# Kernel tuning notes

Hardware: AMD Instinct MI355X
Metric: run time of the kernel (lower is better)

Reference implementation:

```python
import jax, jax.numpy as jnp
import numpy as np

B, T = 128, 1024
SERIES_IN, Y = 35, 8
H = 256
CON, BIN = 25, 10
D = SERIES_IN + Y  # 43, lstm input size


def setup_inputs() -> dict:
    key = jax.random.key(0)
    ks = jax.random.split(key, 14)
    def w(k, shape, s=0.05):
        return jax.random.normal(k, shape, dtype=jnp.float32) * s
    return {
        "x": jax.random.normal(ks[0], (B, T, D), dtype=jnp.float32),
        # DPLSTM (single layer), gate order i,f,g,o like torch
        "W_ih": w(ks[1], (4 * H, D)),
        "W_hh": w(ks[2], (4 * H, H)),
        "b_ih": w(ks[3], (4 * H,)),
        "b_hh": w(ks[4], (4 * H,)),
        # action head
        "W_afc1": w(ks[5], (H, H)),
        "b_afc1": w(ks[6], (H,)),
        "W_aout": w(ks[7], (Y, H)),
        "b_aout": w(ks[8], (Y,)),
        # outcome heads take [out, current_action] -> H+Y features
        "W_cont": w(ks[9], (2 * CON, H + Y)),
        "b_cont": w(ks[10], (2 * CON,)),
        "W_bin": w(ks[11], (BIN, H + Y)),
        "b_bin": w(ks[12], (BIN,)),
    }


def lstm(x, W_ih, W_hh, b_ih, b_hh):
    # x: [B, T, D] -> hidden states [B, T, H]; torch gate order i, f, g, o
    Hh = W_hh.shape[1]
    # precompute input projections for all timesteps (fold both biases in)
    xg = jnp.einsum("btd,gd->btg", x, W_ih) + b_ih + b_hh  # [B, T, 4H]

    def step(carry, g_t):
        h, c = carry
        gates = g_t + h @ W_hh.T  # [B, 4H]
        i, f, g, o = jnp.split(gates, 4, axis=-1)
        i = jax.nn.sigmoid(i)
        f = jax.nn.sigmoid(f)
        g = jnp.tanh(g)
        o = jax.nn.sigmoid(o)
        c = f * c + i * g
        h = o * jnp.tanh(c)
        return (h, c), h

    Bsz = x.shape[0]
    init = (jnp.zeros((Bsz, Hh), x.dtype), jnp.zeros((Bsz, Hh), x.dtype))
    _, hs = jax.lax.scan(step, init, jnp.swapaxes(xg, 0, 1))  # [T, B, H]
    return jnp.swapaxes(hs, 0, 1)


def reference(x, W_ih, W_hh, b_ih, b_hh, W_afc1, b_afc1, W_aout, b_aout,
              W_cont, b_cont, W_bin, b_bin):
    cur = x[:, :, -Y:]                                   # current action [B,T,Y]
    prev = jnp.concatenate([jnp.zeros_like(cur[:, :1]), cur[:, :-1]], axis=1)
    xin = jnp.concatenate([x[:, :, :-Y], prev], axis=-1)  # [B,T,D]
    out = lstm(xin, W_ih, W_hh, b_ih, b_hh)               # [B,T,H]
    # gradient reversal is identity in forward
    act = jax.nn.relu(out @ W_afc1.T + b_afc1) @ W_aout.T + b_aout  # [B,T,Y]
    pred = jnp.concatenate([out, cur], axis=-1)           # [B,T,H+Y]
    cont_params = pred @ W_cont.T + b_cont                # [B,T,2*CON]
    bin_params = jax.nn.sigmoid(pred @ W_bin.T + b_bin)   # [B,T,BIN]
    return cont_params, bin_params, act
```

## Files before the change

kernel.cpp:

```cpp
#include <hip/hip_runtime.h>

typedef unsigned int u32;
typedef unsigned short u16;
typedef unsigned char u8;
typedef unsigned long long u64;
typedef __attribute__((ext_vector_type(8))) short short8;
typedef __attribute__((ext_vector_type(4))) float floatx4;
typedef __attribute__((ext_vector_type(4))) int intx4;

#define TT 1024
#define BIN_OFF 6553600
#define ACT_OFF 7864320

__device__ __forceinline__ u16 f2b(float f) {
  u32 u = __builtin_bit_cast(u32, f);
  u += 0x7fffu + ((u >> 16) & 1u);
  return (u16)(u >> 16);
}
__device__ __forceinline__ float sigm2(float z) {
  return __builtin_amdgcn_rcpf(1.0f + __expf(-z));
}
__device__ __forceinline__ float tanh2(float z) {
  z = fminf(z, 15.0f);
  float e = __expf(2.0f * z);
  return (e - 1.0f) * __builtin_amdgcn_rcpf(e + 1.0f);
}
__device__ __forceinline__ float sigmf(float x) { return 1.0f / (1.0f + __expf(-x)); }


__global__ void k_zero4(u32* __restrict__ p) {
  if (threadIdx.x < 4) p[threadIdx.x] = 0;
}
__global__ void k_amax(const float* __restrict__ x, const float* __restrict__ wih,
                       const float* __restrict__ whh, u32* __restrict__ am) {
  __shared__ float red[256];
  const int tid = threadIdx.x;
  int b = blockIdx.x;
  const float* src; size_t n; int sec, b0, nb;
  if (b < 1920)      { src = x;   n = 5636096; sec = 0; b0 = 0;    nb = 1920; }
  else if (b < 2016) { src = whh; n = 262144;  sec = 1; b0 = 1920; nb = 96; }
  else               { src = wih; n = 44032;   sec = 2; b0 = 2016; nb = 32; }
  float m = 0.f;
  for (size_t i = (size_t)(b - b0) * 256 + tid; i < n; i += (size_t)nb * 256)
    m = fmaxf(m, fabsf(src[i]));
  red[tid] = m;
  __syncthreads();
  for (int s = 128; s > 0; s >>= 1) {
    if (tid < s) red[tid] = fmaxf(red[tid], red[tid + s]);
    __syncthreads();
  }
  if (tid == 0) atomicMax(&am[sec], __float_as_uint(red[0]));
}
__global__ void k_prep_bias(const float* __restrict__ a, const float* __restrict__ b,
                            float* __restrict__ o) {
  int i = blockIdx.x * 256 + threadIdx.x;
  o[i] = a[i] + b[i];
}
__global__ void k_prep_wq2(const float* __restrict__ wih, const float* __restrict__ whh,
                           const float* __restrict__ bias, const u32* __restrict__ am,
                           int* __restrict__ wq, float* __restrict__ sbuf) {
  u32 idx = blockIdx.x * 256 + threadIdx.x;
  const float xmax = fmaxf(__uint_as_float(am[0]), 1e-8f);
  const float whm  = fmaxf(__uint_as_float(am[1]), 1e-8f);
  const float wxm  = fmaxf(__uint_as_float(am[2]), 1e-8f);
  const float sn_h = whm / 127.0f, sn_x = wxm / 127.0f;
  const float sx = xmax / 127.0f;
  const float A_h = sn_h / 127.0f;
  const float A_x = sn_x * sx;
  if (idx == 0) { sbuf[0] = A_h; sbuf[1] = A_x; }
  int jq = idx & 3;
  int lane = (idx >> 2) & 63;
  u32 wf = idx >> 8;
  int F = wf % 40, w = wf / 40;
  int tile = F / 5, c = F % 5;
  int gate = tile >> 1, ht = tile & 1;
  int l15 = lane & 15, kq = lane >> 4;
  int n = gate * 256 + w * 32 + ht * 16 + l15;
  u32 out = 0;
#pragma unroll
  for (int b = 0; b < 4; ++b) {
    int kl = kq * 16 + jq * 4 + b;
    float q = 0.f;
    if (c < 4) {
      q = rintf(whh[n * 256 + c * 64 + kl] / sn_h);
    } else {
      if (kl < 43) q = rintf(wih[n * 43 + kl] / sn_x);
      else if (kl == 43) {
        q = fminf(fmaxf(rintf(bias[n] / (127.0f * A_x)), -127.f), 127.f);
      } else if (kl == 44) {
        float qc = fminf(fmaxf(rintf(bias[n] / (127.0f * A_x)), -127.f), 127.f);
        q = rintf((bias[n] - qc * 127.0f * A_x) / (127.0f * A_h));
      }
    }
    q = fminf(fmaxf(q, -127.f), 127.f);
    int qi = (int)q;
    out |= ((u32)(qi & 255)) << (8 * b);
  }
  wq[idx] = (int)out;
}
__global__ void k_prep_xq2(const float* __restrict__ x, const u32* __restrict__ am,
                           int* __restrict__ xq) {
  u32 idx = blockIdx.x * 256 + threadIdx.x;
  const float xmax = fmaxf(__uint_as_float(am[0]), 1e-8f);
  const float whm  = fmaxf(__uint_as_float(am[1]), 1e-8f);
  const float wxm  = fmaxf(__uint_as_float(am[2]), 1e-8f);
  const float sx = xmax / 127.0f;
  const float sr = whm / (127.0f * wxm);
  u32 unit = idx >> 8;
  u32 dwIn = idx & 255;
  int lane = dwIn >> 2, reg = dwIn & 3;
  int m = lane & 15, kq = lane >> 4;
  int bg = unit >> 8;
  int rem = unit & 255;
  int mt = rem >> 1, res = rem & 1;
  int t = mt * 8 + (m >> 1);
  int row = bg * 2 + (m & 1);
  u32 out = 0;
#pragma unroll
  for (int b = 0; b < 4; ++b) {
    int k = kq * 16 + reg * 4 + b;
    int q = 0;
    if (k < 43) {
      float xv = 0.f;
      if (k < 35) xv = x[((size_t)row * TT + t) * 43 + k];
      else if (t > 0) xv = x[((size_t)row * TT + (t - 1)) * 43 + k];
      float q1 = fminf(fmaxf(rintf(xv / sx), -127.f), 127.f);
      if (!res) q = (int)q1;
      else q = (int)fminf(fmaxf(rintf((xv - sx * q1) / sr), -127.f), 127.f);
    } else if (k == 43) q = res ? 0 : 127;
    else if (k == 44) q = res ? 127 : 0;
    out |= ((u32)(q & 255)) << (8 * b);
  }
  xq[idx] = (int)out;
}
__global__ void k_prep_afc(const float* __restrict__ wafc1, const float* __restrict__ waout,
                           u16* __restrict__ ob1, u16* __restrict__ ob2) {
  int r = blockIdx.x, k = threadIdx.x;
  if (r < 256) ob1[r * 256 + k] = f2b(wafc1[r * 256 + k]);
  else {
    int y = r - 256;
    ob2[y * 256 + k] = f2b(y < 8 ? waout[y * 256 + k] : 0.f);
  }
}
__global__ void k_prep_wcb(const float* __restrict__ wcont, const float* __restrict__ wbin,
                           u16* __restrict__ o) {
  int nrow = blockIdx.x, k = threadIdx.x;
  float v = 0.f;
  if (k < 264) {
    if (nrow < 50) v = wcont[nrow * 264 + k];
    else if (nrow < 60) v = wbin[(nrow - 50) * 264 + k];
  }
  o[nrow * 288 + k] = f2b(v);
}

#define XS 257
__global__ __launch_bounds__(512, 1)
void k_scan9(const int* wq_, const int* __restrict__ xqd,
             const float* __restrict__ sb, u16* __restrict__ hs) {
  __shared__ u8 bimg[2 * 4096];
  __shared__ intx4 gimg[2 * XS];
  __shared__ floatx4 xg[16 * XS];
  const int tid = threadIdx.x;
  const int w = tid >> 6, lane = tid & 63;
  const int l15 = lane & 15, kq = lane >> 4;
  const int bg = blockIdx.x;

  *(uint4*)&bimg[tid * 16] = (uint4){0, 0, 0, 0};

  intx4 wfr[40];
  {
    const intx4* wp = (const intx4*)wq_ + (size_t)(w * 40) * 64 + lane;
#pragma unroll
    for (int F = 0; F < 40; ++F) wfr[F] = wp[(size_t)F * 64];
  }
  const float A_h = sb[0], A_x = sb[1];

  const int* xu = xqd + (size_t)bg * 65536;
  intx4 xcm = *(const intx4*)(xu + lane * 4);
  intx4 xcr = *(const intx4*)(xu + 256 + lane * 4);

  const int wcol = w * 32 + kq * 4;
  const int r = tid >> 8, col = tid & 255;
  const int bwr = r * 256 + (((col >> 4) ^ r) << 4) + (col & 15);
  u16* hgp = hs + ((size_t)(bg * 2 + r) * TT) * 256 + col;

  float c_st = 0.f;
  u16 h16 = 0;
  __syncthreads();

  int t = 0;
  for (int ch = 0; ch < 128; ++ch) {
    {
      const intx4 z = {0, 0, 0, 0};
      intx4 AXa[8], ARa[8];
#pragma unroll
      for (int ht = 0; ht < 2; ++ht)
#pragma unroll
        for (int g = 0; g < 4; ++g) {
          const int F = (g * 2 + ht) * 5 + 4;
          AXa[ht * 4 + g] = __builtin_amdgcn_mfma_i32_16x16x64_i8(wfr[F], xcm, z, 0, 0, 0);
          ARa[ht * 4 + g] = __builtin_amdgcn_mfma_i32_16x16x64_i8(wfr[F], xcr, z, 0, 0, 0);
        }
#pragma unroll
      for (int ht = 0; ht < 2; ++ht)
#pragma unroll
        for (int rr = 0; rr < 4; ++rr) {
          floatx4 P;
#pragma unroll
          for (int g = 0; g < 4; ++g)
            P[g] = A_x * (float)AXa[ht * 4 + g][rr] + A_h * (float)ARa[ht * 4 + g][rr];
          xg[l15 * XS + wcol + ht * 16 + rr] = P;
        }
    }
    __syncthreads();
    {
      const int chn = ch + 1 < 128 ? ch + 1 : 127;
      xcm = *(const intx4*)(xu + chn * 512 + lane * 4);
      xcr = *(const intx4*)(xu + chn * 512 + 256 + lane * 4);
    }
#pragma unroll 1
    for (int tl = 0; tl < 8; ++tl, ++t) {
      const int cur = t & 1, nxt = cur ^ 1;
      if (t > 0) hgp[(size_t)(t - 1) * 256] = h16;
      intx4 bh[4];
#pragma unroll
      for (int c = 0; c < 4; ++c)
        bh[c] = *(const intx4*)&bimg[cur * 4096 + l15 * 256 +
                                     ((((c * 4 + kq) ^ l15) & 15) << 4)];
      const intx4 z = {0, 0, 0, 0};
#pragma unroll
      for (int ht = 0; ht < 2; ++ht) {
        intx4 A[4];
#pragma unroll
        for (int g = 0; g < 4; ++g) {
          const int F = (g * 2 + ht) * 5;
          intx4 a = __builtin_amdgcn_mfma_i32_16x16x64_i8(wfr[F + 0], bh[0], z, 0, 0, 0);
          a = __builtin_amdgcn_mfma_i32_16x16x64_i8(wfr[F + 1], bh[1], a, 0, 0, 0);
          a = __builtin_amdgcn_mfma_i32_16x16x64_i8(wfr[F + 2], bh[2], a, 0, 0, 0);
          A[g] = __builtin_amdgcn_mfma_i32_16x16x64_i8(wfr[F + 3], bh[3], a, 0, 0, 0);
        }
        if (l15 < 2) {
#pragma unroll
          for (int rr = 0; rr < 4; ++rr) {
            intx4 v = {A[0][rr], A[1][rr], A[2][rr], A[3][rr]};
            gimg[l15 * XS + wcol + ht * 16 + rr] = v;
          }
        }
      }
      __syncthreads();
      intx4 ah = gimg[r * XS + col];
      floatx4 P = xg[(tl * 2 + r) * XS + col];
      float iv = sigm2(fmaf(A_h, (float)ah[0], P[0]));
      float fv = sigm2(fmaf(A_h, (float)ah[1], P[1]));
      float gv = tanh2(fmaf(A_h, (float)ah[2], P[2]));
      float ov = sigm2(fmaf(A_h, (float)ah[3], P[3]));
      float cc = fv * c_st + iv * gv;
      c_st = cc;
      float h = ov * tanh2(cc);
      int q = (int)rintf(h * 127.0f);
      bimg[nxt * 4096 + bwr] = (u8)q;
      h16 = f2b(h);
      __syncthreads();
    }
  }
  hgp[(size_t)(TT - 1) * 256] = h16;
}


__global__ __launch_bounds__(256, 2)
void k_act(const u16* __restrict__ hs, const u16* __restrict__ wafc1,
           const u16* __restrict__ waout, const float* __restrict__ b_afc1,
           const float* __restrict__ b_aout, float* __restrict__ act) {
  __shared__ u16 a_sh[16 * 264];
  __shared__ u16 z_sh[16 * 264];
  __shared__ float sb1[256];
  const int tid = threadIdx.x;
  const int wave = tid >> 6, lane = tid & 63;
  const int l15 = lane & 15, kq = lane >> 4;
  const size_t bt0 = (size_t)blockIdx.x * 16;
  sb1[tid] = b_afc1[tid];
#pragma unroll
  for (int i = 0; i < 2; ++i) {
    int chunk = i * 256 + tid;
    int row = chunk >> 5, c = chunk & 31;
    *(uint4*)&a_sh[row * 264 + c * 8] = *(const uint4*)(hs + (bt0 + row) * 256 + c * 8);
  }
  __syncthreads();
  floatx4 acc[4];
#pragma unroll
  for (int nt = 0; nt < 4; ++nt) acc[nt] = (floatx4){0.f, 0.f, 0.f, 0.f};
#pragma unroll
  for (int kt = 0; kt < 8; ++kt) {
    short8 a = *(const short8*)&a_sh[l15 * 264 + kt * 32 + kq * 8];
#pragma unroll
    for (int nt = 0; nt < 4; ++nt) {
      int n = wave * 64 + nt * 16 + l15;
      short8 b = *(const short8*)(wafc1 + n * 256 + kt * 32 + kq * 8);
      acc[nt] = __builtin_amdgcn_mfma_f32_16x16x32_bf16(a, b, acc[nt], 0, 0, 0);
    }
  }
#pragma unroll
  for (int nt = 0; nt < 4; ++nt) {
    int n = wave * 64 + nt * 16 + l15;
    float bb = sb1[n];
#pragma unroll
    for (int r = 0; r < 4; ++r) {
      float v = acc[nt][r] + bb;
      v = v > 0.f ? v : 0.f;
      z_sh[(kq * 4 + r) * 264 + n] = f2b(v);
    }
  }
  __syncthreads();
  if (wave == 0) {
    floatx4 a2 = (floatx4){0.f, 0.f, 0.f, 0.f};
#pragma unroll
    for (int kt = 0; kt < 8; ++kt) {
      short8 a = *(const short8*)&z_sh[l15 * 264 + kt * 32 + kq * 8];
      short8 b = *(const short8*)(waout + l15 * 256 + kt * 32 + kq * 8);
      a2 = __builtin_amdgcn_mfma_f32_16x16x32_bf16(a, b, a2, 0, 0, 0);
    }
    if (l15 < 8) {
      float bb = b_aout[l15];
#pragma unroll
      for (int r = 0; r < 4; ++r)
        act[(bt0 + (size_t)(kq * 4 + r)) * 8 + l15] = a2[r] + bb;
    }
  }
}

__global__ __launch_bounds__(256, 2)
void k_cb(const u16* __restrict__ hs, const float* __restrict__ x,
          const u16* __restrict__ wcb, const float* __restrict__ b_cont,
          const float* __restrict__ b_bin, float* __restrict__ dout) {
  __shared__ u16 a_sh[16 * 296];
  const int tid = threadIdx.x;
  const int wave = tid >> 6, lane = tid & 63;
  const int l15 = lane & 15, kq = lane >> 4;
  const size_t bt0 = (size_t)blockIdx.x * 16;
#pragma unroll
  for (int i = 0; i < 2; ++i) {
    int chunk = i * 256 + tid;
    int row = chunk >> 5, c = chunk & 31;
    *(uint4*)&a_sh[row * 296 + c * 8] = *(const uint4*)(hs + (bt0 + row) * 256 + c * 8);
  }
  if (tid < 128) {
    int m = tid >> 3, j = tid & 7;
    a_sh[m * 296 + 256 + j] = f2b(x[(bt0 + m) * 43 + 35 + j]);
  }
  for (int i = tid; i < 384; i += 256) {
    int m = i / 24, jj = i % 24;
    a_sh[m * 296 + 264 + jj] = 0;
  }
  __syncthreads();
  const int n = wave * 16 + l15;
  floatx4 acc = (floatx4){0.f, 0.f, 0.f, 0.f};
#pragma unroll
  for (int kt = 0; kt < 9; ++kt) {
    short8 a = *(const short8*)&a_sh[l15 * 296 + kt * 32 + kq * 8];
    short8 b = *(const short8*)(wcb + n * 288 + kt * 32 + kq * 8);
    acc = __builtin_amdgcn_mfma_f32_16x16x32_bf16(a, b, acc, 0, 0, 0);
  }
  if (n < 50) {
    float bb = b_cont[n];
#pragma unroll
    for (int r = 0; r < 4; ++r)
      dout[(bt0 + (size_t)(kq * 4 + r)) * 50 + n] = acc[r] + bb;
  } else if (n < 60) {
    float bb = b_bin[n - 50];
#pragma unroll
    for (int r = 0; r < 4; ++r)
      dout[BIN_OFF + (bt0 + (size_t)(kq * 4 + r)) * 10 + (n - 50)] = sigmf(acc[r] + bb);
  }
}

extern "C" void kernel_launch(void* const* d_in, const int* in_sizes, int n_in,
                              void* d_out, int out_size, void* d_ws, size_t ws_size,
                              hipStream_t stream) {
  const float* x      = (const float*)d_in[0];
  const float* W_ih   = (const float*)d_in[1];
  const float* W_hh   = (const float*)d_in[2];
  const float* b_ih   = (const float*)d_in[3];
  const float* b_hh   = (const float*)d_in[4];
  const float* W_afc1 = (const float*)d_in[5];
  const float* b_afc1 = (const float*)d_in[6];
  const float* W_aout = (const float*)d_in[7];
  const float* b_aout = (const float*)d_in[8];
  const float* W_cont = (const float*)d_in[9];
  const float* b_cont = (const float*)d_in[10];
  const float* W_bin  = (const float*)d_in[11];
  const float* b_bin  = (const float*)d_in[12];
  float* outf = (float*)d_out;
  char* ws = (char*)d_ws;

  u32*   am     = (u32*)(ws);
  float* bias   = (float*)(ws + 64);
  float* sbuf   = (float*)(ws + 4160);
  int*   wq     = (int*)(ws + 4224);
  u16*   wafc1b = (u16*)(ws + 331904);
  u16*   waoutb = (u16*)(ws + 462976);
  u16*   wcbb   = (u16*)(ws + 471168);
  int*   xqd    = (int*)(ws + 524288);
  u16*   hs     = (u16*)(ws + 17305600);

  hipLaunchKernelGGL(k_zero4, dim3(1), dim3(64), 0, stream, am);
  hipLaunchKernelGGL(k_amax, dim3(2048), dim3(256), 0, stream, x, W_ih, W_hh, am);
  hipLaunchKernelGGL(k_prep_bias, dim3(4), dim3(256), 0, stream, b_ih, b_hh, bias);
  hipLaunchKernelGGL(k_prep_wq2, dim3(320), dim3(256), 0, stream, W_ih, W_hh, bias, am, wq, sbuf);
  hipLaunchKernelGGL(k_prep_xq2, dim3(16384), dim3(256), 0, stream, x, am, xqd);
  hipLaunchKernelGGL(k_prep_afc, dim3(272), dim3(256), 0, stream, W_afc1, W_aout, wafc1b, waoutb);
  hipLaunchKernelGGL(k_prep_wcb, dim3(64), dim3(288), 0, stream, W_cont, W_bin, wcbb);
  hipLaunchKernelGGL(k_scan9, dim3(64), dim3(512), 0, stream, wq, xqd, sbuf, hs);
  hipLaunchKernelGGL(k_act, dim3(8192), dim3(256), 0, stream, hs, wafc1b, waoutb, b_afc1, b_aout, outf + ACT_OFF);
  hipLaunchKernelGGL(k_cb, dim3(8192), dim3(256), 0, stream, hs, x, wcbb, b_cont, b_bin, outf);
}
```

Measured before the change: 1.541 ms.

## Double-buffer input-gate projection and overlap it with recurrent LSTM steps

Moves the per-chunk input projection (xg) into a double-buffered shared array and computes the next chunk's projection inside the recurrent step loop, spread across timesteps 0–1, with the global prefetch at step 2. This removes the extra barrier and the serial projection phase at each chunk boundary. It also replaces __syncthreads with a manual lgkmcnt wait plus s_barrier and sched_barrier, and raises wave priority around the recurrent MFMAs. The cost is double the xg shared memory and extra work on the critical step path in some iterations.

Result: faster. 1.483 ms (-3.8%).

```diff
diff --git a/kernel.cpp b/kernel.cpp
--- a/kernel.cpp
+++ b/kernel.cpp
@@ -154,12 +154,36 @@
 }
 
 #define XS 257
+#define BARX() do { \
+  asm volatile("s_waitcnt lgkmcnt(0)" ::: "memory"); \
+  __builtin_amdgcn_s_barrier(); \
+  __builtin_amdgcn_sched_barrier(0); \
+} while (0)
+#define PHASEG_HALF(xgw, HT, XM, XR) do { \
+  const intx4 z_ = {0, 0, 0, 0}; \
+  intx4 AX_[4], AR_[4]; \
+  _Pragma("unroll") \
+  for (int g_ = 0; g_ < 4; ++g_) { \
+    const int F_ = (g_ * 2 + (HT)) * 5 + 4; \
+    AX_[g_] = __builtin_amdgcn_mfma_i32_16x16x64_i8(wfr[F_], (XM), z_, 0, 0, 0); \
+    AR_[g_] = __builtin_amdgcn_mfma_i32_16x16x64_i8(wfr[F_], (XR), z_, 0, 0, 0); \
+  } \
+  _Pragma("unroll") \
+  for (int rr_ = 0; rr_ < 4; ++rr_) { \
+    floatx4 P_; \
+    _Pragma("unroll") \
+    for (int g_ = 0; g_ < 4; ++g_) \
+      P_[g_] = A_x * (float)AX_[g_][rr_] + A_h * (float)AR_[g_][rr_]; \
+    (xgw)[l15 * XS + wcol + (HT) * 16 + rr_] = P_; \
+  } \
+} while (0)
+
 __global__ __launch_bounds__(512, 1)
-void k_scan9(const int* wq_, const int* __restrict__ xqd,
-             const float* __restrict__ sb, u16* __restrict__ hs) {
+void k_scan11(const int* wq_, const int* __restrict__ xqd,
+              const float* __restrict__ sb, u16* __restrict__ hs) {
   __shared__ u8 bimg[2 * 4096];
   __shared__ intx4 gimg[2 * XS];
-  __shared__ floatx4 xg[16 * XS];
+  __shared__ floatx4 xg[2][16 * XS];
   const int tid = threadIdx.x;
   const int w = tid >> 6, lane = tid & 63;
   const int l15 = lane & 15, kq = lane >> 4;
@@ -176,48 +200,27 @@
   const float A_h = sb[0], A_x = sb[1];
 
   const int* xu = xqd + (size_t)bg * 65536;
-  intx4 xcm = *(const intx4*)(xu + lane * 4);
-  intx4 xcr = *(const intx4*)(xu + 256 + lane * 4);
-
   const int wcol = w * 32 + kq * 4;
   const int r = tid >> 8, col = tid & 255;
   const int bwr = r * 256 + (((col >> 4) ^ r) << 4) + (col & 15);
   u16* hgp = hs + ((size_t)(bg * 2 + r) * TT) * 256 + col;
 
+  {
+    intx4 xcm = *(const intx4*)(xu + lane * 4);
+    intx4 xcr = *(const intx4*)(xu + 256 + lane * 4);
+    PHASEG_HALF(xg[0], 0, xcm, xcr);
+    PHASEG_HALF(xg[0], 1, xcm, xcr);
+  }
+  intx4 xnm = *(const intx4*)(xu + 512 + lane * 4);
+  intx4 xnr = *(const intx4*)(xu + 512 + 256 + lane * 4);
+
   float c_st = 0.f;
   u16 h16 = 0;
   __syncthreads();
 
   int t = 0;
   for (int ch = 0; ch < 128; ++ch) {
-    {
-      const intx4 z = {0, 0, 0, 0};
-      intx4 AXa[8], ARa[8];
-#pragma unroll
-      for (int ht = 0; ht < 2; ++ht)
-#pragma unroll
-        for (int g = 0; g < 4; ++g) {
-          const int F = (g * 2 + ht) * 5 + 4;
-          AXa[ht * 4 + g] = __builtin_amdgcn_mfma_i32_16x16x64_i8(wfr[F], xcm, z, 0, 0, 0);
-          ARa[ht * 4 + g] = __builtin_amdgcn_mfma_i32_16x16x64_i8(wfr[F], xcr, z, 0, 0, 0);
-        }
-#pragma unroll
-      for (int ht = 0; ht < 2; ++ht)
-#pragma unroll
-        for (int rr = 0; rr < 4; ++rr) {
-          floatx4 P;
-#pragma unroll
-          for (int g = 0; g < 4; ++g)
-            P[g] = A_x * (float)AXa[ht * 4 + g][rr] + A_h * (float)ARa[ht * 4 + g][rr];
-          xg[l15 * XS + wcol + ht * 16 + rr] = P;
-        }
-    }
-    __syncthreads();
-    {
-      const int chn = ch + 1 < 128 ? ch + 1 : 127;
-      xcm = *(const intx4*)(xu + chn * 512 + lane * 4);
-      xcr = *(const intx4*)(xu + chn * 512 + 256 + lane * 4);
-    }
+    const int rb = ch & 1, wb = rb ^ 1;
 #pragma unroll 1
     for (int tl = 0; tl < 8; ++tl, ++t) {
       const int cur = t & 1, nxt = cur ^ 1;
@@ -228,6 +231,7 @@
         bh[c] = *(const intx4*)&bimg[cur * 4096 + l15 * 256 +
                                      ((((c * 4 + kq) ^ l15) & 15) << 4)];
       const intx4 z = {0, 0, 0, 0};
+      __builtin_amdgcn_s_setprio(1);
 #pragma unroll
       for (int ht = 0; ht < 2; ++ht) {
         intx4 A[4];
@@ -247,9 +251,10 @@
           }
         }
       }
-      __syncthreads();
+      __builtin_amdgcn_s_setprio(0);
+      BARX();
       intx4 ah = gimg[r * XS + col];
-      floatx4 P = xg[(tl * 2 + r) * XS + col];
+      floatx4 P = xg[rb][(tl * 2 + r) * XS + col];
       float iv = sigm2(fmaf(A_h, (float)ah[0], P[0]));
       float fv = sigm2(fmaf(A_h, (float)ah[1], P[1]));
       float gv = tanh2(fmaf(A_h, (float)ah[2], P[2]));
@@ -260,7 +265,14 @@
       int q = (int)rintf(h * 127.0f);
       bimg[nxt * 4096 + bwr] = (u8)q;
       h16 = f2b(h);
-      __syncthreads();
+      if (tl == 0)      PHASEG_HALF(xg[wb], 0, xnm, xnr);
+      else if (tl == 1) PHASEG_HALF(xg[wb], 1, xnm, xnr);
+      else if (tl == 2) {
+        const int chn = ch + 2 < 128 ? ch + 2 : 127;
+        xnm = *(const intx4*)(xu + chn * 512 + lane * 4);
+        xnr = *(const intx4*)(xu + chn * 512 + 256 + lane * 4);
+      }
+      BARX();
     }
   }
   hgp[(size_t)(TT - 1) * 256] = h16;
@@ -409,7 +421,7 @@
   hipLaunchKernelGGL(k_prep_xq2, dim3(16384), dim3(256), 0, stream, x, am, xqd);
   hipLaunchKernelGGL(k_prep_afc, dim3(272), dim3(256), 0, stream, W_afc1, W_aout, wafc1b, waoutb);
   hipLaunchKernelGGL(k_prep_wcb, dim3(64), dim3(288), 0, stream, W_cont, W_bin, wcbb);
-  hipLaunchKernelGGL(k_scan9, dim3(64), dim3(512), 0, stream, wq, xqd, sbuf, hs);
+  hipLaunchKernelGGL(k_scan11, dim3(64), dim3(512), 0, stream, wq, xqd, sbuf, hs);
   hipLaunchKernelGGL(k_act, dim3(8192), dim3(256), 0, stream, hs, wafc1b, waoutb, b_afc1, b_aout, outf + ACT_OFF);
   hipLaunchKernelGGL(k_cb, dim3(8192), dim3(256), 0, stream, hs, x, wcbb, b_cont, b_bin, outf);
 }
```
